# Kernel tuning notes

Measured on AMD Instinct MI355X. Metric: run time of the kernel, lower is better.

## Reference

```python
import jax, jax.numpy as jnp
import numpy as np

B, N, M, D = 4, 4096, 4096, 128


def setup_inputs() -> dict:
    key = jax.random.key(0)
    kk, kq, kv = jax.random.split(key, 3)
    return {
        "k": jax.random.normal(kk, (B, N, D), dtype=jnp.float32),
        "q": jax.random.normal(kq, (B, M, D), dtype=jnp.float32),
        "v": jax.random.normal(kv, (B, M, D), dtype=jnp.float32),
    }


def reference(k, q, v):
    # scores: [B, N, M] = k @ q^T
    scores = jnp.einsum("bnd,bmd->bnm", k, q)
    # Original uses nn.Softmax() with no dim; torch's legacy rule resolves
    # dim=0 for 3-D inputs, so softmax is over the batch axis, applied twice.
    w = jax.nn.softmax(jax.nn.softmax(scores, axis=0), axis=0)
    out = jnp.einsum("bnm,bmd->bnd", w, v)
    return out
```

## Files before the change

kernel.cpp:

```cpp
#include <hip/hip_runtime.h>
#include <hip/hip_bf16.h>

#define NB 4
#define NN 4096
#define MM 4096
#define DD 128
#define BN 32
#define BM 64
#define NCH 4
#define OUT_ELEMS ((size_t)NB * NN * DD)

using f32x4  = __attribute__((ext_vector_type(4))) float;
using bf16x8 = __attribute__((ext_vector_type(8))) short;

__device__ __forceinline__ float fast_exp2(float x) {
  return __builtin_amdgcn_exp2f(x);
}

__device__ __forceinline__ int rfl(int x) {
  return __builtin_amdgcn_readfirstlane(x);
}

__device__ __forceinline__ short f2bf(float x) {
  union { __hip_bfloat16 h; short s; } u;
  u.h = __float2bfloat16(x);
  return u.s;
}

__device__ __forceinline__ float bf2f(unsigned short s) {
  union { float f; unsigned u; } u;
  u.u = ((unsigned)s) << 16;
  return u.f;
}

__device__ __forceinline__ bf16x8 pack8(const float* __restrict__ p) {
  float4 a = *(const float4*)p;
  float4 b = *(const float4*)(p + 4);
  bf16x8 r;
  r[0] = f2bf(a.x); r[1] = f2bf(a.y); r[2] = f2bf(a.z); r[3] = f2bf(a.w);
  r[4] = f2bf(b.x); r[5] = f2bf(b.y); r[6] = f2bf(b.z); r[7] = f2bf(b.w);
  return r;
}

__global__ __launch_bounds__(256) void zero_out_kernel(float4* __restrict__ out) {
  out[(size_t)blockIdx.x * 256 + threadIdx.x] = (float4){0.f, 0.f, 0.f, 0.f};
}

__global__ __launch_bounds__(256) void cvt_frag_kernel(const float* __restrict__ s0,
                                                       const float* __restrict__ s1,
                                                       unsigned short* __restrict__ d0,
                                                       unsigned short* __restrict__ d1) {
  const float* src = blockIdx.y ? s1 : s0;
  unsigned short* dst = blockIdx.y ? d1 : d0;
  const int blk = blockIdx.x;
  const int b = blk >> 8, rf = blk & 255;
  const int kf = threadIdx.x >> 6, l = threadIdx.x & 63;
  const int lr = l & 15, hg = l >> 4;
  const float* s = src + ((size_t)(b * 4096 + rf * 16 + lr) * DD + kf * 32 + hg * 8);
  bf16x8 r = pack8(s);
  *(bf16x8*)(dst + (((size_t)((b * 256 + rf) * 4 + kf)) << 9) + (l << 3)) = r;
}

__global__ __launch_bounds__(256) void transpose_v_frag_kernel(const float* __restrict__ v,
                                                               unsigned short* __restrict__ vt) {
  __shared__ unsigned short t[64][72];
  const int b = blockIdx.z, d0 = blockIdx.y * 64, m0 = blockIdx.x * 64;
  const int r = threadIdx.x >> 2, c4 = threadIdx.x & 3;
  const float* src = v + ((size_t)b * MM + m0 + r) * DD + d0 + c4 * 16;
  for (int j = 0; j < 4; ++j) {
    float4 x = *(const float4*)(src + j * 4);
    int dl = c4 * 16 + j * 4;
    t[dl + 0][r] = (unsigned short)f2bf(x.x);
    t[dl + 1][r] = (unsigned short)f2bf(x.y);
    t[dl + 2][r] = (unsigned short)f2bf(x.z);
    t[dl + 3][r] = (unsigned short)f2bf(x.w);
  }
  __syncthreads();
  const int s8 = threadIdx.x >> 5;
  const int dfl = s8 & 3, mtl = s8 >> 2;
  const int t32 = threadIdx.x & 31;
  for (int ll = 0; ll < 2; ++ll) {
    const int l = t32 * 2 + ll;
    const int lr = l & 15, hg = l >> 4;
    bf16x8 val = *(bf16x8*)&t[dfl * 16 + lr][mtl * 32 + hg * 8];
    *(bf16x8*)(vt + (((size_t)((b * 8 + (d0 >> 4) + dfl) * 128 + (m0 >> 5) + mtl)) << 9) +
               (l << 3)) = val;
  }
}

__global__ __launch_bounds__(256) void reduce4_frag_kernel(const unsigned short* __restrict__ p,
                                                           float* __restrict__ out) {
  const size_t idx = (size_t)blockIdx.x * 256 + threadIdx.x;
  float r0 = 0.f, r1 = 0.f, r2 = 0.f, r3 = 0.f;
  for (int c = 0; c < NCH; ++c) {
    ushort4 a = *(const ushort4*)(p + (size_t)c * OUT_ELEMS + idx * 4);
    r0 += bf2f(a.x); r1 += bf2f(a.y); r2 += bf2f(a.z); r3 += bf2f(a.w);
  }
  const int l = (int)(idx & 63);
  const int djg = (int)((idx >> 6) & 7);
  const int nf = (int)((idx >> 9) & 255);
  const int bq = (int)(idx >> 17);
  const int lr = l & 15, hg = l >> 4;
  float* o = out + ((size_t)(bq * 4096 + nf * 16 + hg * 4) * DD + djg * 16 + lr);
  o[0] = r0; o[DD] = r1; o[2 * DD] = r2; o[3 * DD] = r3;
}

#define LGKM0_SBAR()                                        \
  do {                                                      \
    asm volatile("s_waitcnt lgkmcnt(0)" ::: "memory");      \
    __builtin_amdgcn_sched_barrier(0);                      \
    __builtin_amdgcn_s_barrier();                           \
  } while (0)

template <bool WS, bool PART>
__global__ __launch_bounds__(512, 4) void attn_fused(
    const float* __restrict__ k, const float* __restrict__ q, const float* __restrict__ v,
    const unsigned short* __restrict__ kbt, const unsigned short* __restrict__ qbt,
    const unsigned short* __restrict__ vtt, void* __restrict__ outp) {
  __shared__ alignas(8)  unsigned short s_pos[NB][8][64][4];
  __shared__ alignas(16) unsigned short Wl[2][NB][BN][BM];

  const int tid = threadIdx.x;
  const int wv = tid >> 6, l = tid & 63, lr = l & 15, hg = l >> 4;
  const int voff = l << 3;
  const int wg = blockIdx.x;
  const int cid = wg & (NCH - 1);
  const int nt = wg >> 2;
  const int n0 = nt * BN;
  const int it0 = cid * (MM / BM / NCH);
  const int it1 = it0 + (MM / BM / NCH);

  const int bq = wv >> 1, h = wv & 1;
  const int h_s = wv >> 2, fi_s = (wv >> 1) & 1, fj_s = wv & 1;

  bf16x8 ka[2][4];
  {
    const unsigned short* kp = WS ? (kbt + rfl(((bq * 256 + nt * 2) * 4) << 9)) : nullptr;
    for (int fn = 0; fn < 2; ++fn)
      for (int kf = 0; kf < 4; ++kf) {
        if (WS) ka[fn][kf] = *(const bf16x8*)(kp + fn * 2048 + kf * 512 + voff);
        else    ka[fn][kf] = pack8(k + ((size_t)bq * NN + n0 + fn * 16 + lr) * DD +
                                   kf * 32 + hg * 8);
      }
  }

  f32x4 acc[2][4];
  for (int fi = 0; fi < 2; ++fi)
    for (int dj = 0; dj < 4; ++dj) acc[fi][dj] = (f32x4){0.f, 0.f, 0.f, 0.f};

  bf16x8 vf[4][2];
  bf16x8 qf[2][4];
  float  p[NB][4];

  auto load_q = [&](int it) {
    if (WS) {
      const unsigned short* qp = qbt + rfl(((bq * 256 + it * 4 + h * 2) * 4) << 9);
      for (int fm = 0; fm < 2; ++fm)
        for (int kf = 0; kf < 4; ++kf)
          qf[fm][kf] = *(const bf16x8*)(qp + fm * 2048 + kf * 512 + voff);
    } else {
      const int m0 = it * BM;
      for (int fm = 0; fm < 2; ++fm)
        for (int kf = 0; kf < 4; ++kf)
          qf[fm][kf] = pack8(q + ((size_t)bq * MM + m0 + h * 32 + fm * 16 + lr) * DD +
                             kf * 32 + hg * 8);
    }
  };

  auto qk_mfma = [&]() {
    f32x4 s[2][2];
    for (int fm = 0; fm < 2; ++fm)
      for (int fn = 0; fn < 2; ++fn) s[fm][fn] = (f32x4){0.f, 0.f, 0.f, 0.f};
    __builtin_amdgcn_s_setprio(1);
    for (int kf = 0; kf < 4; ++kf)
      for (int fm = 0; fm < 2; ++fm)
        for (int fn = 0; fn < 2; ++fn)
          s[fm][fn] = __builtin_amdgcn_mfma_f32_16x16x32_bf16(qf[fm][kf], ka[fn][kf],
                                                              s[fm][fn], 0, 0, 0);
    __builtin_amdgcn_s_setprio(0);
    for (int fm = 0; fm < 2; ++fm)
      for (int fn = 0; fn < 2; ++fn) {
        short4 pk;
        pk.x = f2bf(s[fm][fn][0]); pk.y = f2bf(s[fm][fn][1]);
        pk.z = f2bf(s[fm][fn][2]); pk.w = f2bf(s[fm][fn][3]);
        *(short4*)&s_pos[bq][h * 4 + fm * 2 + fn][l][0] = pk;
      }
  };

  auto issue_v = [&](int it) {
    if (WS) {
      const unsigned short* vp = vtt + rfl((((bq * 8 + h * 4) * 128) + it * 2) << 9);
      for (int dj = 0; dj < 4; ++dj)
        for (int kf = 0; kf < 2; ++kf)
          vf[dj][kf] = *(const bf16x8*)(vp + dj * 65536 + kf * 512 + voff);
    } else {
      const int m0 = it * BM;
      for (int dj = 0; dj < 4; ++dj)
        for (int kf = 0; kf < 2; ++kf) {
          bf16x8 t;
          for (int e = 0; e < 8; ++e)
            t[e] = f2bf(v[((size_t)bq * MM + m0 + kf * 32 + hg * 8 + e) * DD +
                          h * 64 + dj * 16 + lr]);
          vf[dj][kf] = t;
        }
    }
  };

  auto sm_round1 = [&]() {
    const float L2E = 1.4426950408889634f;
    for (int qq = 0; qq < 4; ++qq) {
      float x0, x1, x2, x3;
      {
        short4 s0 = *(short4*)&s_pos[0][wv][l][0];
        short4 s1 = *(short4*)&s_pos[1][wv][l][0];
        short4 s2 = *(short4*)&s_pos[2][wv][l][0];
        short4 s3 = *(short4*)&s_pos[3][wv][l][0];
        const short* a0 = (const short*)&s0;
        const short* a1 = (const short*)&s1;
        const short* a2 = (const short*)&s2;
        const short* a3 = (const short*)&s3;
        x0 = bf2f((unsigned short)a0[qq]); x1 = bf2f((unsigned short)a1[qq]);
        x2 = bf2f((unsigned short)a2[qq]); x3 = bf2f((unsigned short)a3[qq]);
      }
      float e0 = fast_exp2(x0 * L2E), e1 = fast_exp2(x1 * L2E);
      float e2 = fast_exp2(x2 * L2E), e3 = fast_exp2(x3 * L2E);
      float inv = __builtin_amdgcn_rcpf((e0 + e1) + (e2 + e3)) * L2E;
      p[0][qq] = e0 * inv; p[1][qq] = e1 * inv;
      p[2][qq] = e2 * inv; p[3][qq] = e3 * inv;
    }
  };

  auto sm_round2 = [&](int buf) {
    const int n_loc = fj_s * 16 + lr;
    const int mchunk = (h_s * 4 + fi_s * 2 + (hg >> 1)) ^ (n_loc & 7);
    const int moff = mchunk * 8 + (hg & 1) * 4;
    float w[NB][4];
    for (int qq = 0; qq < 4; ++qq) {
      float f0 = fast_exp2(p[0][qq]), f1 = fast_exp2(p[1][qq]);
      float f2v = fast_exp2(p[2][qq]), f3 = fast_exp2(p[3][qq]);
      float inv2 = __builtin_amdgcn_rcpf((f0 + f1) + (f2v + f3));
      w[0][qq] = f0 * inv2; w[1][qq] = f1 * inv2;
      w[2][qq] = f2v * inv2; w[3][qq] = f3 * inv2;
    }
    for (int bb = 0; bb < NB; ++bb) {
      short4 pk;
      pk.x = f2bf(w[bb][0]); pk.y = f2bf(w[bb][1]);
      pk.z = f2bf(w[bb][2]); pk.w = f2bf(w[bb][3]);
      *(short4*)&Wl[buf][bb][n_loc][moff] = pk;
    }
  };

  auto do_pv = [&](int buf) {
    bf16x8 wf[2][2];
    for (int fi = 0; fi < 2; ++fi)
      for (int kf = 0; kf < 2; ++kf) {
        const int row = fi * 16 + lr, mo = kf * 32 + hg * 8;
        wf[fi][kf] = *(bf16x8*)&Wl[buf][bq][row][mo ^ ((row & 7) << 3)];
      }
    __builtin_amdgcn_s_setprio(1);
    for (int kf = 0; kf < 2; ++kf)
      for (int fi = 0; fi < 2; ++fi)
        for (int dj = 0; dj < 4; ++dj)
          acc[fi][dj] = __builtin_amdgcn_mfma_f32_16x16x32_bf16(wf[fi][kf], vf[dj][kf],
                                                                acc[fi][dj], 0, 0, 0);
    __builtin_amdgcn_s_setprio(0);
  };

  load_q(it0);
  qk_mfma();
  LGKM0_SBAR();
  for (int t = it0; t < it1; ++t) {
    sm_round1();
    LGKM0_SBAR();
    sm_round2(t & 1);
    if (t > it0) do_pv((t - 1) & 1);
    if (t + 1 < it1) {
      load_q(t + 1);
      qk_mfma();
    }
    issue_v(t);
    LGKM0_SBAR();
  }
  do_pv((it1 - 1) & 1);

  if (PART) {
    unsigned short* dst = (unsigned short*)outp + (size_t)cid * OUT_ELEMS +
                          rfl((((bq * 256 + nt * 2) * 8 + h * 4)) << 8);
    for (int fi = 0; fi < 2; ++fi)
      for (int dj = 0; dj < 4; ++dj) {
        short4 pk;
        pk.x = f2bf(acc[fi][dj][0]); pk.y = f2bf(acc[fi][dj][1]);
        pk.z = f2bf(acc[fi][dj][2]); pk.w = f2bf(acc[fi][dj][3]);
        *(short4*)(dst + fi * 2048 + dj * 256 + (l << 2)) = pk;
      }
  } else {
    float* dst = (float*)outp;
    for (int fi = 0; fi < 2; ++fi)
      for (int dj = 0; dj < 4; ++dj)
        for (int qq = 0; qq < 4; ++qq)
          atomicAdd(dst + ((size_t)bq * NN + n0 + fi * 16 + hg * 4 + qq) * DD +
                        h * 64 + dj * 16 + lr,
                    acc[fi][dj][qq]);
  }
}

extern "C" void kernel_launch(void* const* d_in, const int* in_sizes, int n_in,
                              void* d_out, int out_size, void* d_ws, size_t ws_size,
                              hipStream_t stream) {
  (void)in_sizes; (void)n_in; (void)out_size;
  const float* k = (const float*)d_in[0];
  const float* q = (const float*)d_in[1];
  const float* v = (const float*)d_in[2];
  float* out = (float*)d_out;

  const size_t elems = (size_t)NB * MM * DD;
  const size_t need_bf = 3 * elems * sizeof(unsigned short);
  const size_t need_full = need_bf + NCH * OUT_ELEMS * sizeof(unsigned short);
  const bool use_ws = (d_ws != nullptr) && (ws_size >= need_bf);
  const bool use_part = (d_ws != nullptr) && (ws_size >= need_full);

  if (use_ws) {
    unsigned short* kbt = (unsigned short*)d_ws;
    unsigned short* qbt = kbt + elems;
    unsigned short* vtt = qbt + elems;
    cvt_frag_kernel<<<dim3(NB * 256, 2), 256, 0, stream>>>(k, q, kbt, qbt);
    transpose_v_frag_kernel<<<dim3(MM / 64, DD / 64, NB), 256, 0, stream>>>(v, vtt);
    if (use_part) {
      unsigned short* partials = vtt + elems;
      attn_fused<true, true><<<dim3(NN / BN * NCH), 512, 0, stream>>>(k, q, v, kbt, qbt, vtt,
                                                                      (void*)partials);
      reduce4_frag_kernel<<<2048, 256, 0, stream>>>(partials, out);
    } else {
      zero_out_kernel<<<(NB * NN * DD) / 4 / 256, 256, 0, stream>>>((float4*)out);
      attn_fused<true, false><<<dim3(NN / BN * NCH), 512, 0, stream>>>(k, q, v, kbt, qbt, vtt,
                                                                       (void*)out);
    }
  } else {
    zero_out_kernel<<<(NB * NN * DD) / 4 / 256, 256, 0, stream>>>((float4*)out);
    attn_fused<false, false><<<dim3(NN / BN * NCH), 512, 0, stream>>>(k, q, v, nullptr,
                                                                      nullptr, nullptr,
                                                                      (void*)out);
  }
}
```

Measured before the change: 76.11 us.

## Merge prep kernels and relax scheduling barriers and priority hints in attention

Merges the K/Q bf16 fragment conversion and the V transpose into one prep kernel launch, with a 3-row grid where the third row handles V and idles its surplus blocks. The LDS barrier macro drops the sched_barrier and gains a compiler memory fence after the barrier. The s_setprio raises around the MFMA loops are removed. The softmax round-1 LDS loads are hoisted out of the per-element loop. These aim to cut launch overhead and give the compiler more scheduling freedom, at the risk of worse MFMA/VALU interleaving across waves.

```diff
diff --git a/kernel.cpp b/kernel.cpp
--- a/kernel.cpp
+++ b/kernel.cpp
@@ -46,25 +46,26 @@
   out[(size_t)blockIdx.x * 256 + threadIdx.x] = (float4){0.f, 0.f, 0.f, 0.f};
 }
 
-__global__ __launch_bounds__(256) void cvt_frag_kernel(const float* __restrict__ s0,
-                                                       const float* __restrict__ s1,
-                                                       unsigned short* __restrict__ d0,
-                                                       unsigned short* __restrict__ d1) {
-  const float* src = blockIdx.y ? s1 : s0;
-  unsigned short* dst = blockIdx.y ? d1 : d0;
-  const int blk = blockIdx.x;
-  const int b = blk >> 8, rf = blk & 255;
-  const int kf = threadIdx.x >> 6, l = threadIdx.x & 63;
-  const int lr = l & 15, hg = l >> 4;
-  const float* s = src + ((size_t)(b * 4096 + rf * 16 + lr) * DD + kf * 32 + hg * 8);
-  bf16x8 r = pack8(s);
-  *(bf16x8*)(dst + (((size_t)((b * 256 + rf) * 4 + kf)) << 9) + (l << 3)) = r;
-}
-
-__global__ __launch_bounds__(256) void transpose_v_frag_kernel(const float* __restrict__ v,
-                                                               unsigned short* __restrict__ vt) {
+__global__ __launch_bounds__(256) void prep_kernel(
+    const float* __restrict__ k, const float* __restrict__ q, const float* __restrict__ v,
+    unsigned short* __restrict__ kbt, unsigned short* __restrict__ qbt,
+    unsigned short* __restrict__ vtt) {
   __shared__ unsigned short t[64][72];
-  const int b = blockIdx.z, d0 = blockIdx.y * 64, m0 = blockIdx.x * 64;
+  if (blockIdx.y < 2) {
+    const float* src = blockIdx.y ? q : k;
+    unsigned short* dst = blockIdx.y ? qbt : kbt;
+    const int blk = blockIdx.x;
+    const int b = blk >> 8, rf = blk & 255;
+    const int kf = threadIdx.x >> 6, l = threadIdx.x & 63;
+    const int lr = l & 15, hg = l >> 4;
+    const float* s = src + ((size_t)(b * 4096 + rf * 16 + lr) * DD + kf * 32 + hg * 8);
+    *(bf16x8*)(dst + (((size_t)((b * 256 + rf) * 4 + kf)) << 9) + (l << 3)) = pack8(s);
+    return;
+  }
+  if (blockIdx.x >= 512) return;
+  const int b = blockIdx.x >> 7;
+  const int rem = blockIdx.x & 127;
+  const int d0 = (rem >> 6) * 64, m0 = (rem & 63) * 64;
   const int r = threadIdx.x >> 2, c4 = threadIdx.x & 3;
   const float* src = v + ((size_t)b * MM + m0 + r) * DD + d0 + c4 * 16;
   for (int j = 0; j < 4; ++j) {
@@ -83,7 +84,7 @@
     const int l = t32 * 2 + ll;
     const int lr = l & 15, hg = l >> 4;
     bf16x8 val = *(bf16x8*)&t[dfl * 16 + lr][mtl * 32 + hg * 8];
-    *(bf16x8*)(vt + (((size_t)((b * 8 + (d0 >> 4) + dfl) * 128 + (m0 >> 5) + mtl)) << 9) +
+    *(bf16x8*)(vtt + (((size_t)((b * 8 + (d0 >> 4) + dfl) * 128 + (m0 >> 5) + mtl)) << 9) +
                (l << 3)) = val;
   }
 }
@@ -108,8 +109,8 @@
 #define LGKM0_SBAR()                                        \
   do {                                                      \
     asm volatile("s_waitcnt lgkmcnt(0)" ::: "memory");      \
-    __builtin_amdgcn_sched_barrier(0);                      \
     __builtin_amdgcn_s_barrier();                           \
+    asm volatile("" ::: "memory");                          \
   } while (0)
 
 template <bool WS, bool PART>
@@ -171,13 +172,11 @@
     f32x4 s[2][2];
     for (int fm = 0; fm < 2; ++fm)
       for (int fn = 0; fn < 2; ++fn) s[fm][fn] = (f32x4){0.f, 0.f, 0.f, 0.f};
-    __builtin_amdgcn_s_setprio(1);
     for (int kf = 0; kf < 4; ++kf)
       for (int fm = 0; fm < 2; ++fm)
         for (int fn = 0; fn < 2; ++fn)
           s[fm][fn] = __builtin_amdgcn_mfma_f32_16x16x32_bf16(qf[fm][kf], ka[fn][kf],
                                                               s[fm][fn], 0, 0, 0);
-    __builtin_amdgcn_s_setprio(0);
     for (int fm = 0; fm < 2; ++fm)
       for (int fn = 0; fn < 2; ++fn) {
         short4 pk;
@@ -208,22 +207,19 @@
 
   auto sm_round1 = [&]() {
     const float L2E = 1.4426950408889634f;
+    short4 s0 = *(short4*)&s_pos[0][wv][l][0];
+    short4 s1 = *(short4*)&s_pos[1][wv][l][0];
+    short4 s2 = *(short4*)&s_pos[2][wv][l][0];
+    short4 s3 = *(short4*)&s_pos[3][wv][l][0];
+    const short* a0 = (const short*)&s0;
+    const short* a1 = (const short*)&s1;
+    const short* a2 = (const short*)&s2;
+    const short* a3 = (const short*)&s3;
     for (int qq = 0; qq < 4; ++qq) {
-      float x0, x1, x2, x3;
-      {
-        short4 s0 = *(short4*)&s_pos[0][wv][l][0];
-        short4 s1 = *(short4*)&s_pos[1][wv][l][0];
-        short4 s2 = *(short4*)&s_pos[2][wv][l][0];
-        short4 s3 = *(short4*)&s_pos[3][wv][l][0];
-        const short* a0 = (const short*)&s0;
-        const short* a1 = (const short*)&s1;
-        const short* a2 = (const short*)&s2;
-        const short* a3 = (const short*)&s3;
-        x0 = bf2f((unsigned short)a0[qq]); x1 = bf2f((unsigned short)a1[qq]);
-        x2 = bf2f((unsigned short)a2[qq]); x3 = bf2f((unsigned short)a3[qq]);
-      }
-      float e0 = fast_exp2(x0 * L2E), e1 = fast_exp2(x1 * L2E);
-      float e2 = fast_exp2(x2 * L2E), e3 = fast_exp2(x3 * L2E);
+      float e0 = fast_exp2(bf2f((unsigned short)a0[qq]) * L2E);
+      float e1 = fast_exp2(bf2f((unsigned short)a1[qq]) * L2E);
+      float e2 = fast_exp2(bf2f((unsigned short)a2[qq]) * L2E);
+      float e3 = fast_exp2(bf2f((unsigned short)a3[qq]) * L2E);
       float inv = __builtin_amdgcn_rcpf((e0 + e1) + (e2 + e3)) * L2E;
       p[0][qq] = e0 * inv; p[1][qq] = e1 * inv;
       p[2][qq] = e2 * inv; p[3][qq] = e3 * inv;
@@ -257,13 +253,11 @@
         const int row = fi * 16 + lr, mo = kf * 32 + hg * 8;
         wf[fi][kf] = *(bf16x8*)&Wl[buf][bq][row][mo ^ ((row & 7) << 3)];
       }
-    __builtin_amdgcn_s_setprio(1);
     for (int kf = 0; kf < 2; ++kf)
       for (int fi = 0; fi < 2; ++fi)
         for (int dj = 0; dj < 4; ++dj)
           acc[fi][dj] = __builtin_amdgcn_mfma_f32_16x16x32_bf16(wf[fi][kf], vf[dj][kf],
                                                                 acc[fi][dj], 0, 0, 0);
-    __builtin_amdgcn_s_setprio(0);
   };
 
   load_q(it0);
@@ -323,8 +317,7 @@
     unsigned short* kbt = (unsigned short*)d_ws;
     unsigned short* qbt = kbt + elems;
     unsigned short* vtt = qbt + elems;
-    cvt_frag_kernel<<<dim3(NB * 256, 2), 256, 0, stream>>>(k, q, kbt, qbt);
-    transpose_v_frag_kernel<<<dim3(MM / 64, DD / 64, NB), 256, 0, stream>>>(v, vtt);
+    prep_kernel<<<dim3(NB * 256, 3), 256, 0, stream>>>(k, q, v, kbt, qbt, vtt);
     if (use_part) {
       unsigned short* partials = vtt + elems;
       attn_fused<true, true><<<dim3(NN / BN * NCH), 512, 0, stream>>>(k, q, v, kbt, qbt, vtt,
```

Measured after the change: 75.01 us. About the same (-1.4%).
